# Kernel optimization log

Hardware: AMD Instinct MI355X
Metric: run time of the kernel (lower is better)

## Reference

```python
import jax, jax.numpy as jnp
import numpy as np

N_NODES = 100000
N_PER_GRAPH = 200
N_GRAPHS = N_NODES // N_PER_GRAPH
N_EDGES = 400000
F_IN = 37
H = 128          # node_hidden == transformer_hidden == fc_hidden
HEADS = 8
K_SEEDS = 75     # ceil(0.25 * 300) -> PyG GMT defaults


def _lin(key, out_d, in_d):
    kw, kb = jax.random.split(key)
    w = jax.random.normal(kw, (out_d, in_d), jnp.float32) * float(1.0 / np.sqrt(in_d))
    b = jax.random.normal(kb, (out_d,), jnp.float32) * 0.02
    return w, b


def gcn_layer(x, W, b, src, dst, n):
    # PyG GCNConv with add_self_loops and symmetric deg^-1/2 normalization
    h = x @ W.T                                   # [n, out]
    deg = jnp.ones((n,), h.dtype).at[dst].add(1.0)   # in-degree + self loop
    dinv = jax.lax.rsqrt(deg)
    msg = h[src] * (dinv[src] * dinv[dst])[:, None]  # gather + edge normalize
    agg = jnp.zeros_like(h).at[dst].add(msg)         # scatter-add
    agg = agg + h * (dinv * dinv)[:, None]           # self-loop message
    return agg + b


def attn_block(Q, K, V, fo_W, fo_b):
    # MAB core of GMT: multi-head attention (scaled by sqrt(dim_V)) + rFF residual
    B, nq, d = Q.shape
    dh = d // HEADS
    Qh = Q.reshape(B, nq, HEADS, dh)
    Kh = K.reshape(B, K.shape[1], HEADS, dh)
    Vh = V.reshape(B, V.shape[1], HEADS, dh)
    scores = jnp.einsum('bqhd,bkhd->bhqk', Qh, Kh) / jnp.sqrt(jnp.asarray(d, Q.dtype))
    A = jax.nn.softmax(scores, axis=-1)
    O = jnp.einsum('bhqk,bkhd->bqhd', A, Vh).reshape(B, nq, d)
    out = Q + O
    return out + jax.nn.relu(out @ fo_W.T + fo_b)


def setup_inputs() -> dict:
    key = jax.random.key(0)
    k = iter(jax.random.split(key, 64))
    inp = {}
    inp['herg_em'] = jax.random.normal(next(k), (1, 1280), jnp.float32)
    inp['x'] = jax.random.normal(next(k), (N_NODES, F_IN), jnp.float32)
    inp['edge_attr'] = jax.random.normal(next(k), (N_EDGES, 4), jnp.float32)
    inp['mol_rep'] = jax.random.normal(next(k), (N_GRAPHS, 11), jnp.float32)
    for i, in_d in enumerate([F_IN, H, H, H]):
        inp[f'conv_W{i}'], inp[f'conv_b{i}'] = _lin(next(k), H, in_d)
    inp['lin1_W'], inp['lin1_b'] = _lin(next(k), H, H)
    inp['lin2_W'], inp['lin2_b'] = _lin(next(k), H, H)
    inp['S1'] = jax.random.normal(next(k), (1, K_SEEDS, H), jnp.float32) * 0.1
    for p in ['pma1', 'sab', 'pma2']:
        for nm in ['fq', 'k', 'v', 'fo']:
            inp[f'{p}_{nm}_W'], inp[f'{p}_{nm}_b'] = _lin(next(k), H, H)
    inp['S2'] = jax.random.normal(next(k), (1, 1, H), jnp.float32) * 0.1
    inp['herg_lin_W'], inp['herg_lin_b'] = _lin(next(k), H, 1280)
    inp['herg_out_W'], inp['herg_out_b'] = _lin(next(k), H, 2 * H)
    inp['fc0_W'], inp['fc0_b'] = _lin(next(k), H, H)
    inp['sig_W'], inp['sig_b'] = _lin(next(k), 1, H)
    inp['edge_index'] = jax.random.randint(next(k), (2, N_EDGES), 0, N_NODES, dtype=jnp.int32)
    inp['batch'] = jnp.arange(N_NODES, dtype=jnp.int32) // N_PER_GRAPH
    return inp


def reference(herg_em, x, edge_attr, mol_rep,
              conv_W0, conv_b0, conv_W1, conv_b1, conv_W2, conv_b2, conv_W3, conv_b3,
              lin1_W, lin1_b, lin2_W, lin2_b,
              S1, pma1_fq_W, pma1_fq_b, pma1_k_W, pma1_k_b, pma1_v_W, pma1_v_b, pma1_fo_W, pma1_fo_b,
              sab_fq_W, sab_fq_b, sab_k_W, sab_k_b, sab_v_W, sab_v_b, sab_fo_W, sab_fo_b,
              S2, pma2_fq_W, pma2_fq_b, pma2_k_W, pma2_k_b, pma2_v_W, pma2_v_b, pma2_fo_W, pma2_fo_b,
              herg_lin_W, herg_lin_b, herg_out_W, herg_out_b,
              fc0_W, fc0_b, sig_W, sig_b,
              edge_index, batch):
    src, dst = edge_index[0], edge_index[1]
    n = x.shape[0]

    # stacked GCNConv + ReLU
    h = jax.nn.relu(gcn_layer(x, conv_W0, conv_b0, src, dst, n))
    for W, b in ((conv_W1, conv_b1), (conv_W2, conv_b2), (conv_W3, conv_b3)):
        h = jax.nn.relu(gcn_layer(h, W, b, src, dst, n))

    # GraphMultisetTransformer: lin1 -> GMPool_G -> SelfAtt -> GMPool_I -> lin2
    hx = h @ lin1_W.T + lin1_b                     # [N, H]
    B = N_GRAPHS

    # GMPool_G: seeds attend to GCNConv-projected keys/values (dense per graph)
    Q = jnp.broadcast_to(S1, (B, K_SEEDS, H)) @ pma1_fq_W.T + pma1_fq_b
    K = gcn_layer(hx, pma1_k_W, pma1_k_b, src, dst, n).reshape(B, N_PER_GRAPH, H)
    V = gcn_layer(hx, pma1_v_W, pma1_v_b, src, dst, n).reshape(B, N_PER_GRAPH, H)
    xb = attn_block(Q, K, V, pma1_fo_W, pma1_fo_b)     # [B, 75, H]

    # SelfAtt (SAB)
    Q = xb @ sab_fq_W.T + sab_fq_b
    K = xb @ sab_k_W.T + sab_k_b
    V = xb @ sab_v_W.T + sab_v_b
    xb = attn_block(Q, K, V, sab_fo_W, sab_fo_b)       # [B, 75, H]

    # GMPool_I: single seed, Linear keys/values
    Q = jnp.broadcast_to(S2, (B, 1, H)) @ pma2_fq_W.T + pma2_fq_b
    K = xb @ pma2_k_W.T + pma2_k_b
    V = xb @ pma2_v_W.T + pma2_v_b
    xb = attn_block(Q, K, V, pma2_fo_W, pma2_fo_b)     # [B, 1, H]

    out = xb[:, 0, :] @ lin2_W.T + lin2_b              # [B, H]

    # hERG branch
    herg = jax.nn.relu(herg_em @ herg_lin_W.T + herg_lin_b)   # [1, 128]
    herg = jnp.broadcast_to(herg, (B, herg.shape[1]))
    out = jnp.concatenate([out, herg], axis=1)                 # [B, 256]
    out = jax.nn.relu(out @ herg_out_W.T + herg_out_b)
    out = jax.nn.relu(out @ fc0_W.T + fc0_b)                   # dropout = identity (eval)
    return jax.nn.sigmoid(out @ sig_W.T + sig_b)               # [B, 1]
```

## Files before the change

kernel.cpp:

```cpp
#include <hip/hip_runtime.h>
#include <hip/hip_bf16.h>

typedef unsigned short ushort_t;
typedef unsigned int uint_t;
typedef __attribute__((ext_vector_type(8))) short short8;
typedef __attribute__((ext_vector_type(4))) float float4v;

static constexpr int NN  = 100000;
static constexpr int NE  = 400000;
static constexpr int NB  = 500;
static constexpr int NS  = 75;
static constexpr int H   = 128;
static constexpr float SCALE = 0.08838834764831845f;

union U32 { uint_t u; float f; };
__device__ __forceinline__ float bf2f(ushort_t b){ U32 t; t.u = ((uint_t)b) << 16; return t.f; }
__device__ __forceinline__ ushort_t f2bf(float f){
    U32 t; t.f = f;
    uint_t r = t.u + 0x7fffu + ((t.u >> 16) & 1u);
    return (ushort_t)(r >> 16);
}
__device__ __forceinline__ void fma8(float* a, uint4 u, float c){
    a[0] += c * bf2f((ushort_t)(u.x & 0xffff)); a[1] += c * bf2f((ushort_t)(u.x >> 16));
    a[2] += c * bf2f((ushort_t)(u.y & 0xffff)); a[3] += c * bf2f((ushort_t)(u.y >> 16));
    a[4] += c * bf2f((ushort_t)(u.z & 0xffff)); a[5] += c * bf2f((ushort_t)(u.z >> 16));
    a[6] += c * bf2f((ushort_t)(u.w & 0xffff)); a[7] += c * bf2f((ushort_t)(u.w >> 16));
}

__global__ void k_zero_i(int* __restrict__ p, int n){
    int i = blockIdx.x*256 + threadIdx.x;
    if (i < n) p[i] = 0;
}
__global__ void k_hist(int* counts, const int* __restrict__ dst, int e){
    int i = blockIdx.x*256 + threadIdx.x;
    if (i < e) atomicAdd(&counts[dst[i]], 1);
}
__global__ __launch_bounds__(256) void k_scan1(const int* __restrict__ counts,
    int* __restrict__ row_start, int* __restrict__ blockSums,
    float* __restrict__ dinv, float* __restrict__ selfc, int n){
    __shared__ int s[256];
    int t = threadIdx.x, i = blockIdx.x*256 + t;
    int v = (i < n) ? counts[i] : 0;
    s[t] = v; __syncthreads();
    #pragma unroll
    for (int off = 1; off < 256; off <<= 1){
        int add = (t >= off) ? s[t-off] : 0;
        __syncthreads();
        s[t] += add;
        __syncthreads();
    }
    if (i < n){
        row_start[i] = s[t] - v;
        float r = rsqrtf(1.f + (float)v);
        dinv[i] = r; selfc[i] = r*r;
    }
    if (t == 255) blockSums[blockIdx.x] = s[255];
}
__global__ __launch_bounds__(512) void k_scan2(const int* __restrict__ blockSums,
    int* __restrict__ blockOff, int nb){
    __shared__ int s[512];
    int t = threadIdx.x;
    int v = (t < nb) ? blockSums[t] : 0;
    s[t] = v; __syncthreads();
    #pragma unroll
    for (int off = 1; off < 512; off <<= 1){
        int add = (t >= off) ? s[t-off] : 0;
        __syncthreads();
        s[t] += add;
        __syncthreads();
    }
    blockOff[t] = s[t] - v;
}
__global__ void k_scan3(int* __restrict__ row_start, int* __restrict__ cursor,
                        const int* __restrict__ blockOff, int n, int total){
    int i = blockIdx.x*256 + threadIdx.x;
    if (i < n){
        int v = row_start[i] + blockOff[i >> 8];
        row_start[i] = v; cursor[i] = v;
    }
    if (i == 0) row_start[n] = total;
}
__global__ void k_fillcsr(const int* __restrict__ src, const int* __restrict__ dst,
    const float* __restrict__ dinv, int* cursor,
    int* __restrict__ srcs_s, float* __restrict__ ce_s, int e){
    int i = blockIdx.x*256 + threadIdx.x;
    if (i < e){
        int d = dst[i], s = src[i];
        int p = atomicAdd(&cursor[d], 1);
        srcs_s[p] = s;
        ce_s[p] = dinv[s] * dinv[d];
    }
}

struct CvtArgs { const float* w[17]; const float* w0; const float* s1; const float* s2; const float* x37; };
static constexpr int CVT_W   = 17*16384;
static constexpr int CVT_W0  = 8192;
static constexpr int CVT_S1  = 9600;
static constexpr int CVT_S2  = 128;
static constexpr int CVT_X   = NN*64;
__global__ void k_cvt_all(CvtArgs a, ushort_t* __restrict__ wbf, ushort_t* __restrict__ w0bf,
                          ushort_t* __restrict__ s1bf, ushort_t* __restrict__ s2bf,
                          ushort_t* __restrict__ xb64){
    int i = blockIdx.x*256 + threadIdx.x;
    if (i < CVT_W){ int idx = i >> 14, off = i & 16383; wbf[i] = f2bf(a.w[idx][off]); return; }
    i -= CVT_W;
    if (i < CVT_W0){ int r = i >> 6, c = i & 63; w0bf[i] = (c < 37) ? f2bf(a.w0[r*37 + c]) : (ushort_t)0; return; }
    i -= CVT_W0;
    if (i < CVT_S1){ s1bf[i] = f2bf(a.s1[i]); return; }
    i -= CVT_S1;
    if (i < CVT_S2){ s2bf[i] = f2bf(a.s2[i]); return; }
    i -= CVT_S2;
    if (i < CVT_X){ int r = i >> 6, c = i & 63; xb64[i] = (c < 37) ? f2bf(a.x37[(size_t)r*37 + c]) : (ushort_t)0; return; }
}

__global__ __launch_bounds__(256) void k_seedq(
    const ushort_t* __restrict__ s1bf, const ushort_t* __restrict__ s2bf,
    const ushort_t* __restrict__ W1, const float* __restrict__ bias1,
    const ushort_t* __restrict__ W2q, const float* __restrict__ bias2,
    ushort_t* __restrict__ q0, ushort_t* __restrict__ q2,
    const float* __restrict__ hem, const float* __restrict__ hlW,
    const float* __restrict__ hlb, float* __restrict__ hergv)
{
    int blk = blockIdx.x;
    int tid  = threadIdx.x;
    if (blk == 3){
        __shared__ float e[1280];
        for (int i = tid; i < 1280; i += 256) e[i] = hem[i];
        __syncthreads();
        if (tid < 128){
            float acc = 0.f;
            for (int k = 0; k < 1280; ++k) acc += e[k] * hlW[(size_t)tid*1280 + k];
            hergv[tid] = fmaxf(acc + hlb[tid], 0.f);
        }
        return;
    }
    const ushort_t* x = (blk < 2) ? s1bf : s2bf;
    const ushort_t* W = (blk < 2) ? W1 : W2q;
    const float* bias = (blk < 2) ? bias1 : bias2;
    ushort_t* out = (blk < 2) ? q0 : q2;
    int M = (blk < 2) ? NS : 1;
    int base = (blk < 2) ? blk*64 : 0;
    int wid  = tid >> 6;
    int lane = tid & 63;
    int l15  = lane & 15, quad = lane >> 4;
    int row0 = base + wid*16;
    int ar   = row0 + l15; if (ar > M-1) ar = M-1;
    const short* xr = (const short*)(x + (size_t)ar*H) + quad*8;
    float4v acc[8];
    #pragma unroll
    for (int i = 0; i < 8; ++i) acc[i] = (float4v)0.f;
    #pragma unroll
    for (int kc = 0; kc < 4; ++kc){
        short8 a = *(const short8*)(xr + kc*32);
        #pragma unroll
        for (int nt = 0; nt < 8; ++nt){
            short8 b = *(const short8*)((const short*)(W + (size_t)(nt*16 + l15)*H) + kc*32 + quad*8);
            acc[nt] = __builtin_amdgcn_mfma_f32_16x16x32_bf16(a, b, acc[nt], 0, 0, 0);
        }
    }
    #pragma unroll
    for (int nt = 0; nt < 8; ++nt){
        int c = nt*16 + l15;
        float bv = bias[c];
        #pragma unroll
        for (int reg = 0; reg < 4; ++reg){
            int r = row0 + quad*4 + reg;
            if (r >= M) continue;
            out[(size_t)r*H + c] = f2bf(acc[nt][reg] + bv);
        }
    }
}

template<int NOUT2>
__global__ __launch_bounds__(256, 4) void gemm_fo_then(
    const ushort_t* __restrict__ x, int M,
    const ushort_t* __restrict__ Wfo, const float* __restrict__ bfo,
    const ushort_t* __restrict__ W2,
    const float* __restrict__ b20, const float* __restrict__ b21, const float* __restrict__ b22,
    ushort_t* __restrict__ o0, ushort_t* __restrict__ o1, ushort_t* __restrict__ o2,
    float* __restrict__ o32)
{
    __shared__ ushort_t As[64][136];
    const int tid = threadIdx.x, w = tid >> 6, lane = tid & 63;
    const int l15 = lane & 15, quad = lane >> 4;
    const int row0 = blockIdx.x*64 + w*16;
    int ar = row0 + l15; if (ar > M-1) ar = M-1;
    const short* xr = (const short*)(x + (size_t)ar*H) + quad*8;
    {
        float4v acc[8];
        #pragma unroll
        for (int i = 0; i < 8; ++i) acc[i] = (float4v)0.f;
        #pragma unroll
        for (int kc = 0; kc < 4; ++kc){
            short8 a = *(const short8*)(xr + kc*32);
            #pragma unroll
            for (int nt = 0; nt < 8; ++nt){
                short8 b = *(const short8*)((const short*)(Wfo + (size_t)(nt*16 + l15)*H) + kc*32 + quad*8);
                acc[nt] = __builtin_amdgcn_mfma_f32_16x16x32_bf16(a, b, acc[nt], 0, 0, 0);
            }
        }
        #pragma unroll
        for (int nt = 0; nt < 8; ++nt){
            int c = nt*16 + l15;
            float bv = bfo[c];
            #pragma unroll
            for (int reg = 0; reg < 4; ++reg){
                int r = row0 + quad*4 + reg;
                float v = 0.f;
                if (r < M) v = fmaxf(acc[nt][reg] + bv, 0.f) + bf2f(x[(size_t)r*H + c]);
                As[w*16 + quad*4 + reg][c] = f2bf(v);
            }
        }
    }
    __syncthreads();
    #pragma unroll 1
    for (int n = 0; n < NOUT2; ++n){
        float4v o[8];
        #pragma unroll
        for (int i = 0; i < 8; ++i) o[i] = (float4v)0.f;
        #pragma unroll
        for (int kc = 0; kc < 4; ++kc){
            short8 a = *(const short8*)(&As[w*16 + l15][kc*32 + quad*8]);
            #pragma unroll
            for (int nt = 0; nt < 8; ++nt){
                short8 b = *(const short8*)((const short*)(W2 + (size_t)((n*8 + nt)*16 + l15)*H) + kc*32 + quad*8);
                o[nt] = __builtin_amdgcn_mfma_f32_16x16x32_bf16(a, b, o[nt], 0, 0, 0);
            }
        }
        ushort_t* out = (n == 0) ? o0 : ((n == 1) ? o1 : o2);
        const float* bb = (n == 0) ? b20 : ((n == 1) ? b21 : b22);
        #pragma unroll
        for (int nt = 0; nt < 8; ++nt){
            int c = nt*16 + l15;
            float bv = bb[c];
            #pragma unroll
            for (int reg = 0; reg < 4; ++reg){
                int r = row0 + quad*4 + reg;
                if (r >= M) continue;
                float v = o[nt][reg] + bv;
                if (o32 && n == 0) o32[(size_t)r*H + c] = v;
                else               out[(size_t)r*H + c] = f2bf(v);
            }
        }
    }
}

template<int NOUT, int RELU, int STAGE2, int MINW>
__global__ __launch_bounds__(256, MINW) void k_conv_fused3(
    const ushort_t* __restrict__ x,
    const int* __restrict__ row_st, const int* __restrict__ srcs,
    const float* __restrict__ ces, const float* __restrict__ selfc,
    const ushort_t* __restrict__ W, const float* __restrict__ bias0,
// ... 227 lines not shown
                            : (V + (size_t)b*NK*H + h0*16);
    for (int idx = tid; idx < NK*8; idx += 256){
        int key = idx >> 3, p = idx & 7;
        int hh = p >> 2, dl = (p & 3)*4;
        const ushort_t* src = HM ? (Vb + (size_t)key*32 + hh*16 + dl)
                                 : (Vb + (size_t)key*H + hh*16 + dl);
        Vs[hh][dl+0][key] = src[0];
        Vs[hh][dl+1][key] = src[1];
        Vs[hh][dl+2][key] = src[2];
        Vs[hh][dl+3][key] = src[3];
    }
    for (int idx = tid; idx < 2*16*(232-NK); idx += 256){
        int key = NK + idx % (232-NK), r = idx / (232-NK);
        Vs[r>>4][r&15][key] = 0;
    }
    __syncthreads();

    int w = tid >> 6, lane = tid & 63;
    int hh = w >> 1, half = w & 1;
    int h = h0 + hh;
    int l15 = lane & 15, quad = lane >> 4;
    bool klow = (quad < 2);
    int nqt = (nq + 15) >> 4;
    int split = (nqt + 1) >> 1;
    int qt0 = half ? split : 0;
    int qt1 = half ? nqt : split;
    for (int qt = qt0; qt < qt1; ++qt){
        int qr = qt*16 + l15; if (qr > nq-1) qr = nq-1;
        short8 av = *(const short8*)(Q + (size_t)b*qbs + (size_t)qr*H + h*16 + (quad & 1)*8);
        short8 zero8 = (short8)0;
        short8 afrag = klow ? av : zero8;
        float4v s[NKT];
        #pragma unroll
        for (int kt = 0; kt < NKT; ++kt){
            short8 bv = *(const short8*)(&Ks[hh][kt*16 + l15][(quad & 1)*8]);
            short8 bfrag = klow ? bv : zero8;
            s[kt] = __builtin_amdgcn_mfma_f32_16x16x32_bf16(afrag, bfrag, (float4v)0.f, 0, 0, 0);
        }
        float mx[4] = {-1e30f, -1e30f, -1e30f, -1e30f};
        #pragma unroll
        for (int kt = 0; kt < NKT; ++kt){
            if (kt*16 + l15 >= NK){ s[kt][0]=-1e30f; s[kt][1]=-1e30f; s[kt][2]=-1e30f; s[kt][3]=-1e30f; }
            #pragma unroll
            for (int r = 0; r < 4; ++r) mx[r] = fmaxf(mx[r], s[kt][r]);
        }
        #pragma unroll
        for (int off = 1; off < 16; off <<= 1){
            #pragma unroll
            for (int r = 0; r < 4; ++r) mx[r] = fmaxf(mx[r], __shfl_xor(mx[r], off));
        }
        float sum[4] = {0.f, 0.f, 0.f, 0.f};
        #pragma unroll
        for (int kt = 0; kt < NKT; ++kt){
            #pragma unroll
            for (int r = 0; r < 4; ++r){
                float e = __expf((s[kt][r] - mx[r]) * SCALE);
                sum[r] += e;
                Ps[w][quad*4 + r][kt*16 + l15] = f2bf(e);
            }
        }
        #pragma unroll
        for (int off = 1; off < 16; off <<= 1){
            #pragma unroll
            for (int r = 0; r < 4; ++r) sum[r] += __shfl_xor(sum[r], off);
        }
        float4v o = (float4v)0.f;
        #pragma unroll
        for (int kc = 0; kc < NKC; ++kc){
            short8 pa = *(const short8*)(&Ps[w][l15][kc*32 + quad*8]);
            short8 vb = *(const short8*)(&Vs[hh][l15][kc*32 + quad*8]);
            o = __builtin_amdgcn_mfma_f32_16x16x32_bf16(pa, vb, o, 0, 0, 0);
        }
        #pragma unroll
        for (int r = 0; r < 4; ++r){
            int row = qt*16 + quad*4 + r;
            if (row < nq){
                float qv = bf2f(Q[(size_t)b*qbs + (size_t)row*H + h*16 + l15]);
                out[((size_t)b*nq + row)*H + h*16 + l15] = f2bf(qv + o[r] / sum[r]);
            }
        }
    }
}

__global__ __launch_bounds__(256) void k_pma2_final(
    const ushort_t* __restrict__ q2,
    const ushort_t* __restrict__ K,
    const ushort_t* __restrict__ V,
    const ushort_t* __restrict__ p2foW,
    const float* __restrict__ p2fob,
    const ushort_t* __restrict__ lin2W,
    const float* __restrict__ lin2b,
    const float* __restrict__ hergv,
    const float* __restrict__ hoW, const float* __restrict__ hob,
    const float* __restrict__ fcW, const float* __restrict__ fcb,
    const float* __restrict__ sW,  const float* __restrict__ sb,
    float* __restrict__ outp)
{
    int b = blockIdx.x, t = threadIdx.x;
    __shared__ float sc[8][76];
    __shared__ float sumh[8];
    __shared__ ushort_t xa[128];
    __shared__ ushort_t xb3[128];
    __shared__ float tt[128];
    __shared__ float v256[256];
    __shared__ float red[128];

    const ushort_t* Kb = K + (size_t)b*NS*H;
    const ushort_t* Vb = V + (size_t)b*NS*H;

    {
        int h = t >> 5, l32 = t & 31;
        const ushort_t* qr = q2 + h*16;
        for (int k = l32; k < NS; k += 32){
            const ushort_t* kr = Kb + (size_t)k*H + h*16;
            float s = 0.f;
            #pragma unroll
            for (int d = 0; d < 16; ++d) s += bf2f(qr[d]) * bf2f(kr[d]);
            sc[h][k] = s;
        }
    }
    __syncthreads();
    if (t < 128){
        int hh = t >> 4, i = t & 15;
        float mx = -1e30f;
        for (int k = i; k < NS; k += 16) mx = fmaxf(mx, sc[hh][k]);
        #pragma unroll
        for (int off = 1; off < 16; off <<= 1) mx = fmaxf(mx, __shfl_xor(mx, off));
        float sm = 0.f;
        for (int k = i; k < NS; k += 16){
            float e = __expf((sc[hh][k] - mx) * SCALE);
            sc[hh][k] = e;
            sm += e;
        }
        #pragma unroll
        for (int off = 1; off < 16; off <<= 1) sm += __shfl_xor(sm, off);
        if (i == 0) sumh[hh] = sm;
    }
    __syncthreads();
    if (t < 128){
        int hh = t >> 4;
        float o = 0.f;
        for (int k = 0; k < NS; ++k) o += sc[hh][k] * bf2f(Vb[(size_t)k*H + t]);
        xa[t] = f2bf(bf2f(q2[t]) + o / sumh[hh]);
    }
    __syncthreads();
    if (t < 128){
        float a = 0.f;
        const ushort_t* wr = p2foW + (size_t)t*H;
        for (int k = 0; k < H; ++k) a += bf2f(xa[k]) * bf2f(wr[k]);
        xb3[t] = f2bf(fmaxf(a + p2fob[t], 0.f) + bf2f(xa[t]));
    }
    __syncthreads();
    if (t < 128){
        float a = 0.f;
        const ushort_t* wr = lin2W + (size_t)t*H;
        for (int k = 0; k < H; ++k) a += bf2f(xb3[k]) * bf2f(wr[k]);
        v256[t] = a + lin2b[t];
        v256[128 + t] = hergv[t];
    }
    __syncthreads();
    if (t < 128){
        float acc = 0.f;
        const float* wr = hoW + (size_t)t*256;
        for (int k = 0; k < 256; ++k) acc += v256[k] * wr[k];
        tt[t] = fmaxf(acc + hob[t], 0.f);
    }
    __syncthreads();
    if (t < 128){
        float acc = 0.f;
        const float* wr = fcW + (size_t)t*128;
        for (int k = 0; k < 128; ++k) acc += tt[k] * wr[k];
        float uv = fmaxf(acc + fcb[t], 0.f);
        red[t] = uv * sW[t];
    }
    __syncthreads();
    for (int s = 64; s > 0; s >>= 1){
        if (t < s) red[t] += red[t + s];
        __syncthreads();
    }
    if (t == 0){
        float logit = red[0] + sb[0];
        outp[b] = 1.f / (1.f + expf(-logit));
    }
}

extern "C" void kernel_launch(void* const* d_in, const int* in_sizes, int n_in,
                              void* d_out, int out_size, void* d_ws, size_t ws_size,
                              hipStream_t stream)
{
    (void)in_sizes; (void)n_in; (void)out_size; (void)ws_size;
    const float* herg_em = (const float*)d_in[0];
    const float* x_in    = (const float*)d_in[1];
    const float* convW[4] = {(const float*)d_in[4], (const float*)d_in[6], (const float*)d_in[8], (const float*)d_in[10]};
    const float* convB[4] = {(const float*)d_in[5], (const float*)d_in[7], (const float*)d_in[9], (const float*)d_in[11]};
    const float* lin1W = (const float*)d_in[12]; const float* lin1b = (const float*)d_in[13];
    const float* lin2W = (const float*)d_in[14]; const float* lin2b = (const float*)d_in[15];
    const float* S1    = (const float*)d_in[16];
    const float* p1fqW = (const float*)d_in[17]; const float* p1fqb = (const float*)d_in[18];
    const float* p1kW  = (const float*)d_in[19]; const float* p1kb  = (const float*)d_in[20];
    const float* p1vW  = (const float*)d_in[21]; const float* p1vb  = (const float*)d_in[22];
    const float* p1foW = (const float*)d_in[23]; const float* p1fob = (const float*)d_in[24];
    const float* sfqW  = (const float*)d_in[25]; const float* sfqb  = (const float*)d_in[26];
    const float* skW   = (const float*)d_in[27]; const float* skb   = (const float*)d_in[28];
    const float* svW   = (const float*)d_in[29]; const float* svb   = (const float*)d_in[30];
    const float* sfoW  = (const float*)d_in[31]; const float* sfob  = (const float*)d_in[32];
    const float* p2fqW = (const float*)d_in[33]; const float* p2fqb = (const float*)d_in[34];
    const float* p2kW  = (const float*)d_in[35]; const float* p2kb  = (const float*)d_in[36];
    const float* p2vW  = (const float*)d_in[37]; const float* p2vb  = (const float*)d_in[38];
    const float* p2foW = (const float*)d_in[39]; const float* p2fob = (const float*)d_in[40];
    const float* S2    = (const float*)d_in[41];
    const float* hlW   = (const float*)d_in[42]; const float* hlb   = (const float*)d_in[43];
    const float* hoW   = (const float*)d_in[44]; const float* hob   = (const float*)d_in[45];
    const float* fcW   = (const float*)d_in[46]; const float* fcb   = (const float*)d_in[47];
    const float* sW    = (const float*)d_in[48]; const float* sb    = (const float*)d_in[49];
    const int*  ei    = (const int*)d_in[50];
    const int*  esrc  = ei;
    const int*  edst  = ei + NE;
    float* outp = (float*)d_out;

    char* WS = (char*)d_ws;
    int*   counts = (int*)(WS + 0);
    int*   cursor = (int*)(WS + 400384);
    int*   row_st = (int*)(WS + 800768);
    int*   bSums  = (int*)(WS + 1201152);
    int*   bOff   = (int*)(WS + 1203200);
    float* dinv   = (float*)(WS + 1205248);
    float* selfc  = (float*)(WS + 1605632);
    int*   srcs_s = (int*)(WS + 2005632);
    float* ce_s   = (float*)(WS + 3605632);
    ushort_t* wbf = (ushort_t*)(WS + 5205632);
    ushort_t* w0bf= (ushort_t*)(WS + 5762688);
    ushort_t* s1bf= (ushort_t*)(WS + 5779072);
    ushort_t* s2bf= (ushort_t*)(WS + 5798272);
    ushort_t* q0  = (ushort_t*)(WS + 5798528);
    ushort_t* q2  = (ushort_t*)(WS + 5817728);
    float* hergv  = (float*)(WS + 5817984);
    float* l2out  = (float*)(WS + 5818496);
    ushort_t* xb64= (ushort_t*)(WS + 6074496);
    ushort_t* b0  = (ushort_t*)(WS + 18874496);
    ushort_t* b1  = (ushort_t*)(WS + 44474496);
    ushort_t* b2  = (ushort_t*)(WS + 70074496);
    ushort_t* xA  = (ushort_t*)(WS + 95674496);
    ushort_t* xB  = (ushort_t*)(WS + 105275520);
    ushort_t* xQ  = (ushort_t*)(WS + 114876544);
    ushort_t* xK  = (ushort_t*)(WS + 124477568);
    ushort_t* xV  = (ushort_t*)(WS + 134078592);
    (void)l2out;

    const int gN   = (NN + 255)/256;
    const int gE   = (NE + 255)/256;
    const int gC   = (NN + 31)/32;
    const int gXb  = (NB*NS + 63)/64;

    k_zero_i<<<gN, 256, 0, stream>>>(counts, NN);
    k_hist  <<<gE, 256, 0, stream>>>(counts, edst, NE);
    k_scan1 <<<gN, 256, 0, stream>>>(counts, row_st, bSums, dinv, selfc, NN);
    k_scan2 <<<1, 512, 0, stream>>>(bSums, bOff, gN);
    k_scan3 <<<gN, 256, 0, stream>>>(row_st, cursor, bOff, NN, NE);
    k_fillcsr<<<gE, 256, 0, stream>>>(esrc, edst, dinv, cursor, srcs_s, ce_s, NE);

    CvtArgs ca;
    ca.w[0]=convW[1]; ca.w[1]=convW[2]; ca.w[2]=convW[3]; ca.w[3]=lin1W; ca.w[4]=lin2W;
    ca.w[5]=p1kW; ca.w[6]=p1vW; ca.w[7]=p1foW;
    ca.w[8]=sfqW; ca.w[9]=skW; ca.w[10]=svW; ca.w[11]=sfoW;
    ca.w[12]=p2kW; ca.w[13]=p2vW; ca.w[14]=p2foW; ca.w[15]=p1fqW; ca.w[16]=p2fqW;
    ca.w0 = convW[0]; ca.s1 = S1; ca.s2 = S2; ca.x37 = x_in;
    const int cvtTotal = CVT_W + CVT_W0 + CVT_S1 + CVT_S2 + CVT_X;
    k_cvt_all<<<(cvtTotal + 255)/256, 256, 0, stream>>>(ca, wbf, w0bf, s1bf, s2bf, xb64);

    k_seedq<<<4, 256, 0, stream>>>(s1bf, s2bf, wbf + (size_t)15*16384, p1fqb,
                                   wbf + (size_t)16*16384, p2fqb, q0, q2,
                                   herg_em, hlW, hlb, hergv);

    k_conv0b<<<gC, 256, 0, stream>>>(xb64, row_st, srcs_s, ce_s, selfc, w0bf, convB[0], b0);
    k_conv_fused3<8,1,0,8><<<gC, 256, 0, stream>>>(b0, row_st, srcs_s, ce_s, selfc,
        wbf + (size_t)0*16384, convB[1], nullptr, nullptr, nullptr, b1, nullptr);
    k_conv_fused3<8,1,0,8><<<gC, 256, 0, stream>>>(b1, row_st, srcs_s, ce_s, selfc,
        wbf + (size_t)1*16384, convB[2], nullptr, nullptr, nullptr, b0, nullptr);
    k_conv_fused3<8,1,1,8><<<gC, 256, 0, stream>>>(b0, row_st, srcs_s, ce_s, selfc,
        wbf + (size_t)2*16384, convB[3], nullptr, wbf + (size_t)3*16384, lin1b, b1, nullptr);
    k_conv_fused3<16,0,0,4><<<gC, 256, 0, stream>>>(b1, row_st, srcs_s, ce_s, selfc,
        wbf + (size_t)5*16384, p1kb, p1vb, nullptr, nullptr, b2, b0);
    k_attn_mfma<200,1><<<NB*4, 256, 0, stream>>>(q0, 0, b2, b0, xA, NS);
    gemm_fo_then<3><<<gXb, 256, 0, stream>>>(xA, NB*NS, wbf + (size_t)7*16384, p1fob,
        wbf + (size_t)8*16384, sfqb, skb, svb, xQ, xK, xV, nullptr);
    k_attn_mfma<75,0><<<NB*4, 256, 0, stream>>>(xQ, NS*H, xK, xV, xB, NS);
    gemm_fo_then<2><<<gXb, 256, 0, stream>>>(xB, NB*NS, wbf + (size_t)11*16384, sfob,
        wbf + (size_t)12*16384, p2kb, p2vb, nullptr, xK, xV, nullptr, nullptr);
    k_pma2_final<<<NB, 256, 0, stream>>>(q2, xK, xV,
        wbf + (size_t)14*16384, p2fob, wbf + (size_t)4*16384, lin2b,
        hergv, hoW, hob, fcW, fcb, sW, sb, outp);
}
```

Before: 777.8 us.

## Merge preprocessing kernels and final stage into persistent kernels with grid barriers

Replaces the chain of small preprocessing launches (zero, histogram, three-pass scan, CSR fill, conversion, seed projections, hERG) with a single 512-block kernel that separates phases with a software grid barrier. It also fuses the last fo/keys-values GEMM with the PMA2 and MLP head kernel, again joined by a grid barrier. The aim is to remove launch gaps and idle tails between many short dependent kernels. The risk is deadlock if not all blocks are co-resident, plus the cost of the barriers and lower parallelism in grid-stride loops.

```diff
diff --git a/kernel.cpp b/kernel.cpp
--- a/kernel.cpp
+++ b/kernel.cpp
@@ -11,6 +11,7 @@
 static constexpr int NB  = 500;
 static constexpr int NS  = 75;
 static constexpr int H   = 128;
+static constexpr int GN  = (NN + 255)/256;
 static constexpr float SCALE = 0.08838834764831845f;
 
 union U32 { uint_t u; float f; };
@@ -27,147 +28,170 @@
     a[6] += c * bf2f((ushort_t)(u.w & 0xffff)); a[7] += c * bf2f((ushort_t)(u.w >> 16));
 }
 
-__global__ void k_zero_i(int* __restrict__ p, int n){
-    int i = blockIdx.x*256 + threadIdx.x;
-    if (i < n) p[i] = 0;
-}
-__global__ void k_hist(int* counts, const int* __restrict__ dst, int e){
-    int i = blockIdx.x*256 + threadIdx.x;
-    if (i < e) atomicAdd(&counts[dst[i]], 1);
-}
-__global__ __launch_bounds__(256) void k_scan1(const int* __restrict__ counts,
-    int* __restrict__ row_start, int* __restrict__ blockSums,
-    float* __restrict__ dinv, float* __restrict__ selfc, int n){
-    __shared__ int s[256];
-    int t = threadIdx.x, i = blockIdx.x*256 + t;
-    int v = (i < n) ? counts[i] : 0;
-    s[t] = v; __syncthreads();
-    #pragma unroll
-    for (int off = 1; off < 256; off <<= 1){
-        int add = (t >= off) ? s[t-off] : 0;
-        __syncthreads();
-        s[t] += add;
-        __syncthreads();
-    }
-    if (i < n){
-        row_start[i] = s[t] - v;
-        float r = rsqrtf(1.f + (float)v);
-        dinv[i] = r; selfc[i] = r*r;
-    }
-    if (t == 255) blockSums[blockIdx.x] = s[255];
-}
-__global__ __launch_bounds__(512) void k_scan2(const int* __restrict__ blockSums,
-    int* __restrict__ blockOff, int nb){
-    __shared__ int s[512];
-    int t = threadIdx.x;
-    int v = (t < nb) ? blockSums[t] : 0;
-    s[t] = v; __syncthreads();
-    #pragma unroll
-    for (int off = 1; off < 512; off <<= 1){
-        int add = (t >= off) ? s[t-off] : 0;
-        __syncthreads();
-        s[t] += add;
-        __syncthreads();
-    }
-    blockOff[t] = s[t] - v;
-}
-__global__ void k_scan3(int* __restrict__ row_start, int* __restrict__ cursor,
-                        const int* __restrict__ blockOff, int n, int total){
-    int i = blockIdx.x*256 + threadIdx.x;
-    if (i < n){
-        int v = row_start[i] + blockOff[i >> 8];
-        row_start[i] = v; cursor[i] = v;
-    }
-    if (i == 0) row_start[n] = total;
-}
-__global__ void k_fillcsr(const int* __restrict__ src, const int* __restrict__ dst,
-    const float* __restrict__ dinv, int* cursor,
-    int* __restrict__ srcs_s, float* __restrict__ ce_s, int e){
-    int i = blockIdx.x*256 + threadIdx.x;
-    if (i < e){
-        int d = dst[i], s = src[i];
-        int p = atomicAdd(&cursor[d], 1);
-        srcs_s[p] = s;
-        ce_s[p] = dinv[s] * dinv[d];
-    }
-}
-
-struct CvtArgs { const float* w[17]; const float* w0; const float* s1; const float* s2; const float* x37; };
+__device__ __forceinline__ void gridbar(int* bar, int nblk){
+    __threadfence();
+    __syncthreads();
+    if (threadIdx.x == 0){
+        int g = __hip_atomic_load(&bar[1], __ATOMIC_RELAXED, __HIP_MEMORY_SCOPE_AGENT);
+        int v = __hip_atomic_fetch_add(&bar[0], 1, __ATOMIC_ACQ_REL, __HIP_MEMORY_SCOPE_AGENT);
+        if (v == nblk - 1){
+            __hip_atomic_store(&bar[0], 0, __ATOMIC_RELAXED, __HIP_MEMORY_SCOPE_AGENT);
+            __hip_atomic_fetch_add(&bar[1], 1, __ATOMIC_RELEASE, __HIP_MEMORY_SCOPE_AGENT);
+        } else {
+            while (__hip_atomic_load(&bar[1], __ATOMIC_ACQUIRE, __HIP_MEMORY_SCOPE_AGENT) == g)
+                __builtin_amdgcn_s_sleep(2);
+        }
+        __threadfence();
+    }
+    __syncthreads();
+}
+
 static constexpr int CVT_W   = 17*16384;
 static constexpr int CVT_W0  = 8192;
 static constexpr int CVT_S1  = 9600;
 static constexpr int CVT_S2  = 128;
 static constexpr int CVT_X   = NN*64;
-__global__ void k_cvt_all(CvtArgs a, ushort_t* __restrict__ wbf, ushort_t* __restrict__ w0bf,
-                          ushort_t* __restrict__ s1bf, ushort_t* __restrict__ s2bf,
-                          ushort_t* __restrict__ xb64){
-    int i = blockIdx.x*256 + threadIdx.x;
-    if (i < CVT_W){ int idx = i >> 14, off = i & 16383; wbf[i] = f2bf(a.w[idx][off]); return; }
-    i -= CVT_W;
-    if (i < CVT_W0){ int r = i >> 6, c = i & 63; w0bf[i] = (c < 37) ? f2bf(a.w0[r*37 + c]) : (ushort_t)0; return; }
-    i -= CVT_W0;
-    if (i < CVT_S1){ s1bf[i] = f2bf(a.s1[i]); return; }
-    i -= CVT_S1;
-    if (i < CVT_S2){ s2bf[i] = f2bf(a.s2[i]); return; }
-    i -= CVT_S2;
-    if (i < CVT_X){ int r = i >> 6, c = i & 63; xb64[i] = (c < 37) ? f2bf(a.x37[(size_t)r*37 + c]) : (ushort_t)0; return; }
-}
-
-__global__ __launch_bounds__(256) void k_seedq(
-    const ushort_t* __restrict__ s1bf, const ushort_t* __restrict__ s2bf,
-    const ushort_t* __restrict__ W1, const float* __restrict__ bias1,
-    const ushort_t* __restrict__ W2q, const float* __restrict__ bias2,
-    ushort_t* __restrict__ q0, ushort_t* __restrict__ q2,
-    const float* __restrict__ hem, const float* __restrict__ hlW,
-    const float* __restrict__ hlb, float* __restrict__ hergv)
-{
-    int blk = blockIdx.x;
-    int tid  = threadIdx.x;
-    if (blk == 3){
-        __shared__ float e[1280];
-        for (int i = tid; i < 1280; i += 256) e[i] = hem[i];
-        __syncthreads();
-        if (tid < 128){
-            float acc = 0.f;
-            for (int k = 0; k < 1280; ++k) acc += e[k] * hlW[(size_t)tid*1280 + k];
-            hergv[tid] = fmaxf(acc + hlb[tid], 0.f);
-        }
-        return;
-    }
-    const ushort_t* x = (blk < 2) ? s1bf : s2bf;
-    const ushort_t* W = (blk < 2) ? W1 : W2q;
-    const float* bias = (blk < 2) ? bias1 : bias2;
-    ushort_t* out = (blk < 2) ? q0 : q2;
-    int M = (blk < 2) ? NS : 1;
-    int base = (blk < 2) ? blk*64 : 0;
-    int wid  = tid >> 6;
-    int lane = tid & 63;
-    int l15  = lane & 15, quad = lane >> 4;
-    int row0 = base + wid*16;
-    int ar   = row0 + l15; if (ar > M-1) ar = M-1;
-    const short* xr = (const short*)(x + (size_t)ar*H) + quad*8;
-    float4v acc[8];
-    #pragma unroll
-    for (int i = 0; i < 8; ++i) acc[i] = (float4v)0.f;
-    #pragma unroll
-    for (int kc = 0; kc < 4; ++kc){
-        short8 a = *(const short8*)(xr + kc*32);
-        #pragma unroll
-        for (int nt = 0; nt < 8; ++nt){
-            short8 b = *(const short8*)((const short*)(W + (size_t)(nt*16 + l15)*H) + kc*32 + quad*8);
-            acc[nt] = __builtin_amdgcn_mfma_f32_16x16x32_bf16(a, b, acc[nt], 0, 0, 0);
-        }
-    }
-    #pragma unroll
-    for (int nt = 0; nt < 8; ++nt){
-        int c = nt*16 + l15;
-        float bv = bias[c];
-        #pragma unroll
-        for (int reg = 0; reg < 4; ++reg){
-            int r = row0 + quad*4 + reg;
-            if (r >= M) continue;
-            out[(size_t)r*H + c] = f2bf(acc[nt][reg] + bv);
-        }
+static constexpr int CVT_TOT = CVT_W + CVT_W0 + CVT_S1 + CVT_S2 + CVT_X;
+
+struct PreArgs {
+    int* counts; int* cursor; int* row_st; int* bSums; int* bOff;
+    float* dinv; float* selfc; int* srcs_s; float* ce_s;
+    const int* esrc; const int* edst;
+    const float* w[17]; const float* w0; const float* s1; const float* s2; const float* x37;
+    ushort_t* wbf; ushort_t* w0bf; ushort_t* s1bf; ushort_t* s2bf; ushort_t* xb64;
+    const float* p1fqb; const float* p2fqb; ushort_t* q0; ushort_t* q2;
+    const float* hem; const float* hlW; const float* hlb; float* hergv;
+    int* bar;
+};
+
+__global__ __launch_bounds__(256, 2) void k_pre(PreArgs a){
+    __shared__ float shf[1344];
+    const int tid  = threadIdx.x;
+    const int gtid = blockIdx.x*256 + tid;
+    const int gsz  = gridDim.x*256;
+    const int nblk = gridDim.x;
+
+    for (int i = gtid; i < NN; i += gsz) a.counts[i] = 0;
+    for (int j = gtid; j < CVT_TOT; j += gsz){
+        int i = j;
+        if (i < CVT_W){ int idx = i >> 14, off = i & 16383; a.wbf[i] = f2bf(a.w[idx][off]); continue; }
+        i -= CVT_W;
+        if (i < CVT_W0){ int r = i >> 6, c = i & 63; a.w0bf[i] = (c < 37) ? f2bf(a.w0[r*37 + c]) : (ushort_t)0; continue; }
+        i -= CVT_W0;
+        if (i < CVT_S1){ a.s1bf[i] = f2bf(a.s1[i]); continue; }
+        i -= CVT_S1;
+        if (i < CVT_S2){ a.s2bf[i] = f2bf(a.s2[i]); continue; }
+        i -= CVT_S2;
+        { int r = i >> 6, c = i & 63; a.xb64[i] = (c < 37) ? f2bf(a.x37[(size_t)r*37 + c]) : (ushort_t)0; }
+    }
+    gridbar(a.bar, nblk);
+
+    for (int i = gtid; i < NE; i += gsz) atomicAdd(&a.counts[a.edst[i]], 1);
+    gridbar(a.bar, nblk);
+
+    for (int u = blockIdx.x; u < GN + 4; u += gridDim.x){
+        if (u < GN){
+            int* si = (int*)shf;
+            int i = u*256 + tid;
+            int v = (i < NN) ? a.counts[i] : 0;
+            si[tid] = v; __syncthreads();
+            #pragma unroll
+            for (int off = 1; off < 256; off <<= 1){
+                int add = (tid >= off) ? si[tid-off] : 0;
+                __syncthreads();
+                si[tid] += add;
+                __syncthreads();
+            }
+            if (i < NN){
+                a.row_st[i] = si[tid] - v;
+                float r = rsqrtf(1.f + (float)v);
+                a.dinv[i] = r; a.selfc[i] = r*r;
+            }
+            if (tid == 255) a.bSums[u] = si[255];
+            __syncthreads();
+        } else {
+            int blk = u - GN;
+            if (blk == 3){
+                float* e = shf;
+                for (int i = tid; i < 1280; i += 256) e[i] = a.hem[i];
+                __syncthreads();
+                if (tid < 128){
+                    float acc = 0.f;
+                    for (int k = 0; k < 1280; ++k) acc += e[k] * a.hlW[(size_t)tid*1280 + k];
+                    a.hergv[tid] = fmaxf(acc + a.hlb[tid], 0.f);
+                }
+                __syncthreads();
+            } else {
+                const ushort_t* x = (blk < 2) ? a.s1bf : a.s2bf;
+                const ushort_t* W = (blk < 2) ? (a.wbf + (size_t)15*16384) : (a.wbf + (size_t)16*16384);
+                const float* bias = (blk < 2) ? a.p1fqb : a.p2fqb;
+                ushort_t* out = (blk < 2) ? a.q0 : a.q2;
+                int M = (blk < 2) ? NS : 1;
+                int base = (blk < 2) ? blk*64 : 0;
+                int wid  = tid >> 6;
+                int lane = tid & 63;
+                int l15  = lane & 15, quad = lane >> 4;
+                int row0 = base + wid*16;
+                int ar   = row0 + l15; if (ar > M-1) ar = M-1;
+                const short* xr = (const short*)(x + (size_t)ar*H) + quad*8;
+                float4v acc[8];
+                #pragma unroll
+                for (int i = 0; i < 8; ++i) acc[i] = (float4v)0.f;
+                #pragma unroll
+                for (int kc = 0; kc < 4; ++kc){
+                    short8 av = *(const short8*)(xr + kc*32);
+                    #pragma unroll
+                    for (int nt = 0; nt < 8; ++nt){
+                        short8 bv = *(const short8*)((const short*)(W + (size_t)(nt*16 + l15)*H) + kc*32 + quad*8);
+                        acc[nt] = __builtin_amdgcn_mfma_f32_16x16x32_bf16(av, bv, acc[nt], 0, 0, 0);
+                    }
+                }
+                #pragma unroll
+                for (int nt = 0; nt < 8; ++nt){
+                    int c = nt*16 + l15;
+                    float bv = bias[c];
+                    #pragma unroll
+                    for (int reg = 0; reg < 4; ++reg){
+                        int r = row0 + quad*4 + reg;
+                        if (r >= M) continue;
+                        out[(size_t)r*H + c] = f2bf(acc[nt][reg] + bv);
+                    }
+                }
+            }
+        }
+    }
+    gridbar(a.bar, nblk);
+
+    if (blockIdx.x == 0){
+        int* s2 = (int*)shf;
+        s2[tid]       = (tid < GN) ? a.bSums[tid] : 0;
+        s2[tid + 256] = (tid + 256 < GN) ? a.bSums[tid + 256] : 0;
+        int v0 = s2[tid], v1 = s2[tid + 256];
+        __syncthreads();
+        for (int off = 1; off < 512; off <<= 1){
+            int a0 = (tid >= off) ? s2[tid - off] : 0;
+            int a1 = (tid + 256 >= off) ? s2[tid + 256 - off] : 0;
+            __syncthreads();
+            s2[tid] += a0; s2[tid + 256] += a1;
+            __syncthreads();
+        }
+        if (tid < GN) a.bOff[tid] = s2[tid] - v0;
+        if (tid + 256 < GN) a.bOff[tid + 256] = s2[tid + 256] - v1;
+    }
+    gridbar(a.bar, nblk);
+
+    for (int i = gtid; i < NN; i += gsz){
+        int v = a.row_st[i] + a.bOff[i >> 8];
+        a.row_st[i] = v; a.cursor[i] = v;
+    }
+    if (gtid == 0) a.row_st[NN] = NE;
+    gridbar(a.bar, nblk);
+
+    for (int i = gtid; i < NE; i += gsz){
+        int d = a.edst[i], s = a.esrc[i];
+        int p = atomicAdd(&a.cursor[d], 1);
+        a.srcs_s[p] = s;
+        a.ce_s[p] = a.dinv[s] * a.dinv[d];
     }
 }
 
@@ -561,105 +585,171 @@
     }
 }
 
-__global__ __launch_bounds__(256) void k_pma2_final(
+__global__ __launch_bounds__(256, 4) void k_gft2_final(
+    const ushort_t* __restrict__ x, int M,
+    const ushort_t* __restrict__ Wfo, const float* __restrict__ bfo,
+    const ushort_t* __restrict__ W2,
+    const float* __restrict__ b20, const float* __restrict__ b21,
+    ushort_t* __restrict__ o0, ushort_t* __restrict__ o1,
     const ushort_t* __restrict__ q2,
-    const ushort_t* __restrict__ K,
-    const ushort_t* __restrict__ V,
-    const ushort_t* __restrict__ p2foW,
-    const float* __restrict__ p2fob,
-    const ushort_t* __restrict__ lin2W,
-    const float* __restrict__ lin2b,
+    const ushort_t* __restrict__ p2foW, const float* __restrict__ p2fob,
+    const ushort_t* __restrict__ lin2W, const float* __restrict__ lin2b,
     const float* __restrict__ hergv,
     const float* __restrict__ hoW, const float* __restrict__ hob,
     const float* __restrict__ fcW, const float* __restrict__ fcb,
-    const float* __restrict__ sW,  const float* __restrict__ sb,
-    float* __restrict__ outp)
+    const float* __restrict__ sWv, const float* __restrict__ sbv,
+    float* __restrict__ outp, int* bar)
 {
-    int b = blockIdx.x, t = threadIdx.x;
-    __shared__ float sc[8][76];
-    __shared__ float sumh[8];
-    __shared__ ushort_t xa[128];
-    __shared__ ushort_t xb3[128];
-    __shared__ float tt[128];
-    __shared__ float v256[256];
-    __shared__ float red[128];
-
-    const ushort_t* Kb = K + (size_t)b*NS*H;
-    const ushort_t* Vb = V + (size_t)b*NS*H;
-
+    __shared__ ushort_t As[64][136];
+    const int tid = threadIdx.x, w = tid >> 6, lane = tid & 63;
+    const int l15 = lane & 15, quad = lane >> 4;
     {
-        int h = t >> 5, l32 = t & 31;
-        const ushort_t* qr = q2 + h*16;
-        for (int k = l32; k < NS; k += 32){
-            const ushort_t* kr = Kb + (size_t)k*H + h*16;
-            float s = 0.f;
-            #pragma unroll
-            for (int d = 0; d < 16; ++d) s += bf2f(qr[d]) * bf2f(kr[d]);
-            sc[h][k] = s;
-        }
-    }
-    __syncthreads();
-    if (t < 128){
-        int hh = t >> 4, i = t & 15;
-        float mx = -1e30f;
-        for (int k = i; k < NS; k += 16) mx = fmaxf(mx, sc[hh][k]);
-        #pragma unroll
-        for (int off = 1; off < 16; off <<= 1) mx = fmaxf(mx, __shfl_xor(mx, off));
-        float sm = 0.f;
-        for (int k = i; k < NS; k += 16){
-            float e = __expf((sc[hh][k] - mx) * SCALE);
-            sc[hh][k] = e;
-            sm += e;
-        }
-        #pragma unroll
-        for (int off = 1; off < 16; off <<= 1) sm += __shfl_xor(sm, off);
-        if (i == 0) sumh[hh] = sm;
-    }
-    __syncthreads();
-    if (t < 128){
-        int hh = t >> 4;
-        float o = 0.f;
-        for (int k = 0; k < NS; ++k) o += sc[hh][k] * bf2f(Vb[(size_t)k*H + t]);
-        xa[t] = f2bf(bf2f(q2[t]) + o / sumh[hh]);
-    }
-    __syncthreads();
-    if (t < 128){
-        float a = 0.f;
-        const ushort_t* wr = p2foW + (size_t)t*H;
-        for (int k = 0; k < H; ++k) a += bf2f(xa[k]) * bf2f(wr[k]);
-        xb3[t] = f2bf(fmaxf(a + p2fob[t], 0.f) + bf2f(xa[t]));
-    }
-    __syncthreads();
-    if (t < 128){
-        float a = 0.f;
-        const ushort_t* wr = lin2W + (size_t)t*H;
-        for (int k = 0; k < H; ++k) a += bf2f(xb3[k]) * bf2f(wr[k]);
-        v256[t] = a + lin2b[t];
-        v256[128 + t] = hergv[t];
-    }
-    __syncthreads();
-    if (t < 128){
-        float acc = 0.f;
-        const float* wr = hoW + (size_t)t*256;
-        for (int k = 0; k < 256; ++k) acc += v256[k] * wr[k];
-        tt[t] = fmaxf(acc + hob[t], 0.f);
-    }
-    __syncthreads();
-    if (t < 128){
-        float acc = 0.f;
-        const float* wr = fcW + (size_t)t*128;
-        for (int k = 0; k < 128; ++k) acc += tt[k] * wr[k];
-        float uv = fmaxf(acc + fcb[t], 0.f);
-        red[t] = uv * sW[t];
-    }
-    __syncthreads();
-    for (int s = 64; s > 0; s >>= 1){
-        if (t < s) red[t] += red[t + s];
-        __syncthreads();
-    }
-    if (t == 0){
-        float logit = red[0] + sb[0];
-        outp[b] = 1.f / (1.f + expf(-logit));
+        const int row0 = blockIdx.x*64 + w*16;
+        int ar = row0 + l15; if (ar > M-1) ar = M-1;
+        const short* xr = (const short*)(x + (size_t)ar*H) + quad*8;
+        {
+            float4v acc[8];
+            #pragma unroll
+            for (int i = 0; i < 8; ++i) acc[i] = (float4v)0.f;
+            #pragma unroll
+            for (int kc = 0; kc < 4; ++kc){
+                short8 a = *(const short8*)(xr + kc*32);
+                #pragma unroll
+                for (int nt = 0; nt < 8; ++nt){
+                    short8 b = *(const short8*)((const short*)(Wfo + (size_t)(nt*16 + l15)*H) + kc*32 + quad*8);
+                    acc[nt] = __builtin_amdgcn_mfma_f32_16x16x32_bf16(a, b, acc[nt], 0, 0, 0);
+                }
+            }
+            #pragma unroll
+            for (int nt = 0; nt < 8; ++nt){
+                int c = nt*16 + l15;
+                float bv = bfo[c];
+                #pragma unroll
+                for (int reg = 0; reg < 4; ++reg){
+                    int r = row0 + quad*4 + reg;
+                    float v = 0.f;
+                    if (r < M) v = fmaxf(acc[nt][reg] + bv, 0.f) + bf2f(x[(size_t)r*H + c]);
+                    As[w*16 + quad*4 + reg][c] = f2bf(v);
+                }
+            }
+        }
+        __syncthreads();
+        #pragma unroll 1
+        for (int n = 0; n < 2; ++n){
+            float4v o[8];
+            #pragma unroll
+            for (int i = 0; i < 8; ++i) o[i] = (float4v)0.f;
+            #pragma unroll
+            for (int kc = 0; kc < 4; ++kc){
+                short8 a = *(const short8*)(&As[w*16 + l15][kc*32 + quad*8]);
+                #pragma unroll
+                for (int nt = 0; nt < 8; ++nt){
+                    short8 b = *(const short8*)((const short*)(W2 + (size_t)((n*8 + nt)*16 + l15)*H) + kc*32 + quad*8);
+                    o[nt] = __builtin_amdgcn_mfma_f32_16x16x32_bf16(a, b, o[nt], 0, 0, 0);
+                }
+            }
+            ushort_t* out = (n == 0) ? o0 : o1;
+            const float* bb = (n == 0) ? b20 : b21;
+            #pragma unroll
+            for (int nt = 0; nt < 8; ++nt){
+                int c = nt*16 + l15;
+                float bv = bb[c];
+                #pragma unroll
+                for (int reg = 0; reg < 4; ++reg){
+                    int r = row0 + quad*4 + reg;
+                    if (r >= M) continue;
+                    out[(size_t)r*H + c] = f2bf(o[nt][reg] + bv);
+                }
+            }
+        }
+    }
+    gridbar(bar, gridDim.x);
+    if (blockIdx.x < NB){
+        int b = blockIdx.x, t = tid;
+        char* sb8 = (char*)&As[0][0];
+        float* sc       = (float*)sb8;
+        float* sumh     = (float*)(sb8 + 2432);
+        ushort_t* xa    = (ushort_t*)(sb8 + 2464);
+        ushort_t* xb3   = (ushort_t*)(sb8 + 2720);
+        float* tt       = (float*)(sb8 + 2976);
+        float* v256     = (float*)(sb8 + 3488);
+        float* red      = (float*)(sb8 + 4512);
+        const ushort_t* Kb = o0 + (size_t)b*NS*H;
+        const ushort_t* Vb = o1 + (size_t)b*NS*H;
+        {
+            int h = t >> 5, l32 = t & 31;
+            const ushort_t* qr = q2 + h*16;
+            for (int k = l32; k < NS; k += 32){
+                const ushort_t* kr = Kb + (size_t)k*H + h*16;
+                float s = 0.f;
+                #pragma unroll
+                for (int d = 0; d < 16; ++d) s += bf2f(qr[d]) * bf2f(kr[d]);
+                sc[h*76 + k] = s;
+            }
+        }
+        __syncthreads();
+        if (t < 128){
+            int hh = t >> 4, i = t & 15;
+            float mx = -1e30f;
+            for (int k = i; k < NS; k += 16) mx = fmaxf(mx, sc[hh*76 + k]);
+            #pragma unroll
+            for (int off = 1; off < 16; off <<= 1) mx = fmaxf(mx, __shfl_xor(mx, off));
+            float sm = 0.f;
+            for (int k = i; k < NS; k += 16){
+                float e = __expf((sc[hh*76 + k] - mx) * SCALE);
+                sc[hh*76 + k] = e;
+                sm += e;
+            }
+            #pragma unroll
+            for (int off = 1; off < 16; off <<= 1) sm += __shfl_xor(sm, off);
+            if (i == 0) sumh[hh] = sm;
+        }
+        __syncthreads();
+        if (t < 128){
+            int hh = t >> 4;
+            float o = 0.f;
+            for (int k = 0; k < NS; ++k) o += sc[hh*76 + k] * bf2f(Vb[(size_t)k*H + t]);
+            xa[t] = f2bf(bf2f(q2[t]) + o / sumh[hh]);
+        }
+        __syncthreads();
+        if (t < 128){
+            float a = 0.f;
+            const ushort_t* wr = p2foW + (size_t)t*H;
+            for (int k = 0; k < H; ++k) a += bf2f(xa[k]) * bf2f(wr[k]);
+            xb3[t] = f2bf(fmaxf(a + p2fob[t], 0.f) + bf2f(xa[t]));
+        }
+        __syncthreads();
+        if (t < 128){
+            float a = 0.f;
+            const ushort_t* wr = lin2W + (size_t)t*H;
+            for (int k = 0; k < H; ++k) a += bf2f(xb3[k]) * bf2f(wr[k]);
+            v256[t] = a + lin2b[t];
+            v256[128 + t] = hergv[t];
+        }
+        __syncthreads();
+        if (t < 128){
+            float acc = 0.f;
+            const float* wr = hoW + (size_t)t*256;
+            for (int k = 0; k < 256; ++k) acc += v256[k] * wr[k];
+            tt[t] = fmaxf(acc + hob[t], 0.f);
+        }
+        __syncthreads();
+        if (t < 128){
+            float acc = 0.f;
+            const float* wr = fcW + (size_t)t*128;
+            for (int k = 0; k < 128; ++k) acc += tt[k] * wr[k];
+            float uv = fmaxf(acc + fcb[t], 0.f);
+            red[t] = uv * sWv[t];
+        }
+        __syncthreads();
+        for (int s = 64; s > 0; s >>= 1){
+            if (t < s) red[t] += red[t + s];
+            __syncthreads();
+        }
+        if (t == 0){
+            float logit = red[0] + sbv[0];
+            outp[b] = 1.f / (1.f + expf(-logit));
+        }
     }
 }
 
@@ -699,6 +789,7 @@
 
     char* WS = (char*)d_ws;
     int*   counts = (int*)(WS + 0);
+    int*   bar    = (int*)(WS + 400000);
     int*   cursor = (int*)(WS + 400384);
     int*   row_st = (int*)(WS + 800768);
     int*   bSums  = (int*)(WS + 1201152);
@@ -714,7 +805,6 @@
     ushort_t* q0  = (ushort_t*)(WS + 5798528);
     ushort_t* q2  = (ushort_t*)(WS + 5817728);
     float* hergv  = (float*)(WS + 5817984);
-    float* l2out  = (float*)(WS + 5818496);
     ushort_t* xb64= (ushort_t*)(WS + 6074496);
     ushort_t* b0  = (ushort_t*)(WS + 18874496);
     ushort_t* b1  = (ushort_t*)(WS + 44474496);
@@ -724,32 +814,26 @@
     ushort_t* xQ  = (ushort_t*)(WS + 114876544);
     ushort_t* xK  = (ushort_t*)(WS + 124477568);
     ushort_t* xV  = (ushort_t*)(WS + 134078592);
-    (void)l2out;
-
-    const int gN   = (NN + 255)/256;
-    const int gE   = (NE + 255)/256;
+
     const int gC   = (NN + 31)/32;
     const int gXb  = (NB*NS + 63)/64;
 
-    k_zero_i<<<gN, 256, 0, stream>>>(counts, NN);
-    k_hist  <<<gE, 256, 0, stream>>>(counts, edst, NE);
-    k_scan1 <<<gN, 256, 0, stream>>>(counts, row_st, bSums, dinv, selfc, NN);
-    k_scan2 <<<1, 512, 0, stream>>>(bSums, bOff, gN);
-    k_scan3 <<<gN, 256, 0, stream>>>(row_st, cursor, bOff, NN, NE);
-    k_fillcsr<<<gE, 256, 0, stream>>>(esrc, edst, dinv, cursor, srcs_s, ce_s, NE);
-
-    CvtArgs ca;
-    ca.w[0]=convW[1]; ca.w[1]=convW[2]; ca.w[2]=convW[3]; ca.w[3]=lin1W; ca.w[4]=lin2W;
-    ca.w[5]=p1kW; ca.w[6]=p1vW; ca.w[7]=p1foW;
-    ca.w[8]=sfqW; ca.w[9]=skW; ca.w[10]=svW; ca.w[11]=sfoW;
-    ca.w[12]=p2kW; ca.w[13]=p2vW; ca.w[14]=p2foW; ca.w[15]=p1fqW; ca.w[16]=p2fqW;
-    ca.w0 = convW[0]; ca.s1 = S1; ca.s2 = S2; ca.x37 = x_in;
-    const int cvtTotal = CVT_W + CVT_W0 + CVT_S1 + CVT_S2 + CVT_X;
-    k_cvt_all<<<(cvtTotal + 255)/256, 256, 0, stream>>>(ca, wbf, w0bf, s1bf, s2bf, xb64);
-
-    k_seedq<<<4, 256, 0, stream>>>(s1bf, s2bf, wbf + (size_t)15*16384, p1fqb,
-                                   wbf + (size_t)16*16384, p2fqb, q0, q2,
-                                   herg_em, hlW, hlb, hergv);
+    hipMemsetAsync(bar, 0, 16, stream);
+
+    PreArgs pa;
+    pa.counts = counts; pa.cursor = cursor; pa.row_st = row_st; pa.bSums = bSums; pa.bOff = bOff;
+    pa.dinv = dinv; pa.selfc = selfc; pa.srcs_s = srcs_s; pa.ce_s = ce_s;
+    pa.esrc = esrc; pa.edst = edst;
+    pa.w[0]=convW[1]; pa.w[1]=convW[2]; pa.w[2]=convW[3]; pa.w[3]=lin1W; pa.w[4]=lin2W;
+    pa.w[5]=p1kW; pa.w[6]=p1vW; pa.w[7]=p1foW;
+    pa.w[8]=sfqW; pa.w[9]=skW; pa.w[10]=svW; pa.w[11]=sfoW;
+    pa.w[12]=p2kW; pa.w[13]=p2vW; pa.w[14]=p2foW; pa.w[15]=p1fqW; pa.w[16]=p2fqW;
+    pa.w0 = convW[0]; pa.s1 = S1; pa.s2 = S2; pa.x37 = x_in;
+    pa.wbf = wbf; pa.w0bf = w0bf; pa.s1bf = s1bf; pa.s2bf = s2bf; pa.xb64 = xb64;
+    pa.p1fqb = p1fqb; pa.p2fqb = p2fqb; pa.q0 = q0; pa.q2 = q2;
+    pa.hem = herg_em; pa.hlW = hlW; pa.hlb = hlb; pa.hergv = hergv;
+    pa.bar = bar;
+    k_pre<<<512, 256, 0, stream>>>(pa);
 
     k_conv0b<<<gC, 256, 0, stream>>>(xb64, row_st, srcs_s, ce_s, selfc, w0bf, convB[0], b0);
     k_conv_fused3<8,1,0,8><<<gC, 256, 0, stream>>>(b0, row_st, srcs_s, ce_s, selfc,
@@ -764,9 +848,8 @@
     gemm_fo_then<3><<<gXb, 256, 0, stream>>>(xA, NB*NS, wbf + (size_t)7*16384, p1fob,
         wbf + (size_t)8*16384, sfqb, skb, svb, xQ, xK, xV, nullptr);
     k_attn_mfma<75,0><<<NB*4, 256, 0, stream>>>(xQ, NS*H, xK, xV, xB, NS);
-    gemm_fo_then<2><<<gXb, 256, 0, stream>>>(xB, NB*NS, wbf + (size_t)11*16384, sfob,
-        wbf + (size_t)12*16384, p2kb, p2vb, nullptr, xK, xV, nullptr, nullptr);
-    k_pma2_final<<<NB, 256, 0, stream>>>(q2, xK, xV,
-        wbf + (size_t)14*16384, p2fob, wbf + (size_t)4*16384, lin2b,
-        hergv, hoW, hob, fcW, fcb, sW, sb, outp);
-}
+    k_gft2_final<<<gXb, 256, 0, stream>>>(xB, NB*NS, wbf + (size_t)11*16384, sfob,
+        wbf + (size_t)12*16384, p2kb, p2vb, xK, xV,
+        q2, wbf + (size_t)14*16384, p2fob, wbf + (size_t)4*16384, lin2b,
+        hergv, hoW, hob, fcW, fcb, sW, sb, outp, bar + 2);
+}
```

New measurement: 1.599 ms. 106% more time.
